# Kernel tuning notes

Measured on AMD Instinct MI355X. Metric: run time of the kernel, lower is better.

Reference implementation:

```python
import jax, jax.numpy as jnp
import numpy as np
from jax import lax

KH, KW = 2, 2  # kernel_size
SH, SW = 2, 2  # stride (defaults to kernel_size)


def setup_inputs() -> dict:
    key = jax.random.key(0)
    x = jax.random.normal(key, (16, 96, 224, 224), dtype=jnp.float32)
    return {"x": x}


def reference(x):
    # Max pooling 2D over NCHW, VALID padding:
    # out_h = (H - KH)//SH + 1, out_w = (W - KW)//SW + 1
    neg_inf = jnp.array(-jnp.inf, dtype=x.dtype)
    out = lax.reduce_window(
        x,
        neg_inf,
        lax.max,
        window_dimensions=(1, 1, KH, KW),
        window_strides=(1, 1, SH, SW),
        padding="VALID",
    )
    return out
```

## Files before the change

kernel.cpp:

```cpp
#include <hip/hip_runtime.h>


#define N_  16
#define C_  96
#define H_  224
#define W_  224
#define OH_ 112
#define OW_ 112

__global__ __launch_bounds__(256) void maxpool2d_k(
    const float* __restrict__ x, float* __restrict__ y, int total_quads) {
    int t = blockIdx.x * blockDim.x + threadIdx.x;
    if (t >= total_quads) return;

    int q = t % 28;
    int r = t / 28;
    int oh = r % OH_;
    int nc = r / OH_;

    const float* row0 = x + ((size_t)nc * H_ + (size_t)(2 * oh)) * W_ + q * 8;
    const float* row1 = row0 + W_;

    float4 a0 = *(const float4*)(row0);
    float4 a1 = *(const float4*)(row0 + 4);
    float4 b0 = *(const float4*)(row1);
    float4 b1 = *(const float4*)(row1 + 4);

    float4 o;
    o.x = fmaxf(fmaxf(a0.x, a0.y), fmaxf(b0.x, b0.y));
    o.y = fmaxf(fmaxf(a0.z, a0.w), fmaxf(b0.z, b0.w));
    o.z = fmaxf(fmaxf(a1.x, a1.y), fmaxf(b1.x, b1.y));
    o.w = fmaxf(fmaxf(a1.z, a1.w), fmaxf(b1.z, b1.w));

    *(float4*)(y + (size_t)r * OW_ + q * 4) = o;
}

extern "C" void kernel_launch(void* const* d_in, const int* in_sizes, int n_in,
                              void* d_out, int out_size, void* d_ws, size_t ws_size,
                              hipStream_t stream) {
    const float* x = (const float*)d_in[0];
    float* y = (float*)d_out;

    const int total_quads = N_ * C_ * OH_ * (OW_ / 4);
    const int block = 256;
    const int grid = (total_quads + block - 1) / block;

    maxpool2d_k<<<grid, block, 0, stream>>>(x, y, total_quads);
}
```

Before: 415.2 us.

## Use nontemporal loads/stores and halve per-thread work to two outputs

Each thread now computes two outputs from one 16-byte load per input row instead of four outputs from two loads per row. This doubles the thread count and makes adjacent lanes read contiguous 16-byte chunks. Loads and stores use nontemporal builtins to avoid polluting the cache on this streaming kernel. The cost is more threads and index arithmetic per output, plus narrower 8-byte stores.

```diff
diff --git a/kernel.cpp b/kernel.cpp
--- a/kernel.cpp
+++ b/kernel.cpp
@@ -1,5 +1,8 @@
 #include <hip/hip_runtime.h>
 
+
+typedef float fvec4 __attribute__((ext_vector_type(4)));
+typedef float fvec2 __attribute__((ext_vector_type(2)));
 
 #define N_  16
 #define C_  96
@@ -7,32 +10,30 @@
 #define W_  224
 #define OH_ 112
 #define OW_ 112
+#define PAIRS_PER_ROW (OW_ / 2)
 
 __global__ __launch_bounds__(256) void maxpool2d_k(
-    const float* __restrict__ x, float* __restrict__ y, int total_quads) {
+    const float* __restrict__ x, float* __restrict__ y, int total_pairs) {
     int t = blockIdx.x * blockDim.x + threadIdx.x;
-    if (t >= total_quads) return;
+    if (t >= total_pairs) return;
 
-    int q = t % 28;
-    int r = t / 28;
+    int p  = t % PAIRS_PER_ROW;
+    int r  = t / PAIRS_PER_ROW;
     int oh = r % OH_;
     int nc = r / OH_;
 
-    const float* row0 = x + ((size_t)nc * H_ + (size_t)(2 * oh)) * W_ + q * 8;
-    const float* row1 = row0 + W_;
+    const fvec4* row0 = (const fvec4*)(x + ((size_t)nc * H_ + (size_t)(2 * oh)) * W_) + p;
+    const fvec4* row1 = row0 + (W_ / 4);
 
-    float4 a0 = *(const float4*)(row0);
-    float4 a1 = *(const float4*)(row0 + 4);
-    float4 b0 = *(const float4*)(row1);
-    float4 b1 = *(const float4*)(row1 + 4);
+    fvec4 a = __builtin_nontemporal_load(row0);
+    fvec4 b = __builtin_nontemporal_load(row1);
 
-    float4 o;
-    o.x = fmaxf(fmaxf(a0.x, a0.y), fmaxf(b0.x, b0.y));
-    o.y = fmaxf(fmaxf(a0.z, a0.w), fmaxf(b0.z, b0.w));
-    o.z = fmaxf(fmaxf(a1.x, a1.y), fmaxf(b1.x, b1.y));
-    o.w = fmaxf(fmaxf(a1.z, a1.w), fmaxf(b1.z, b1.w));
+    fvec2 o;
+    o.x = fmaxf(fmaxf(a.x, a.y), fmaxf(b.x, b.y));
+    o.y = fmaxf(fmaxf(a.z, a.w), fmaxf(b.z, b.w));
 
-    *(float4*)(y + (size_t)r * OW_ + q * 4) = o;
+    fvec2* dst = (fvec2*)(y + (size_t)r * OW_) + p;
+    __builtin_nontemporal_store(o, dst);
 }
 
 extern "C" void kernel_launch(void* const* d_in, const int* in_sizes, int n_in,
@@ -41,9 +42,9 @@
     const float* x = (const float*)d_in[0];
     float* y = (float*)d_out;
 
-    const int total_quads = N_ * C_ * OH_ * (OW_ / 4);
+    const int total_pairs = N_ * C_ * OH_ * PAIRS_PER_ROW;
     const int block = 256;
-    const int grid = (total_quads + block - 1) / block;
+    const int grid = (total_pairs + block - 1) / block;
 
-    maxpool2d_k<<<grid, block, 0, stream>>>(x, y, total_quads);
+    maxpool2d_k<<<grid, block, 0, stream>>>(x, y, total_pairs);
 }
```

Result: faster. 399.8 us (-3.7%).
